# Optimization experiments

Measured on AMD Instinct MI355X. Metric: run time of the kernel, lower is better.

Reference implementation:

```python
import jax, jax.numpy as jnp
import numpy as np

N_NODES = 100000
N_EDGES = 1600000
N_GRAPHS = 256
IN_F = 64   # global_features (GNN input dim)
OUT_F = 64  # node_features (GNN output dim)


def setup_inputs() -> dict:
    key = jax.random.key(0)
    ks = jax.random.split(key, 8)
    x = jax.random.normal(ks[0], (N_NODES, IN_F), dtype=jnp.float32)
    edge_index = jax.random.randint(ks[1], (2, N_EDGES), 0, N_NODES, dtype=jnp.int64)
    batch = jnp.sort(jax.random.randint(ks[2], (N_NODES,), 0, N_GRAPHS, dtype=jnp.int64))
    # GNNLayer linear: in=global_features, out=node_features
    W_gnn = jax.random.normal(ks[3], (IN_F, OUT_F), dtype=jnp.float32) / np.sqrt(IN_F)
    b_gnn = jnp.zeros((OUT_F,), dtype=jnp.float32)
    # global_attention: Linear(node_features, 1)
    W_att = jax.random.normal(ks[4], (OUT_F, 1), dtype=jnp.float32) / np.sqrt(OUT_F)
    b_att = jnp.zeros((1,), dtype=jnp.float32)
    return {"x": x, "edge_index": edge_index, "batch": batch,
            "W_gnn": W_gnn, "b_gnn": b_gnn, "W_att": W_att, "b_att": b_att}


def reference(x, edge_index, batch, W_gnn, b_gnn, W_att, b_att):
    src, dst = edge_index[0], edge_index[1]
    # --- GNN message passing layer: aggregate neighbor features, transform ---
    agg = jax.ops.segment_sum(x[src], dst, num_segments=N_NODES)  # [N, IN_F]
    h = jax.nn.relu((x + agg) @ W_gnn + b_gnn)                    # [N, OUT_F]
    # --- attention scores + scatter softmax over batch segments ---
    scores = (h @ W_att + b_att)[:, 0]                            # [N]
    seg_max = jax.ops.segment_max(scores, batch, num_segments=N_GRAPHS)
    e = jnp.exp(scores - seg_max[batch])
    denom = jax.ops.segment_sum(e, batch, num_segments=N_GRAPHS)
    w = e / denom[batch]                                          # [N]
    # --- weighted scatter-add pooling ---
    out = jax.ops.segment_sum(w[:, None] * h, batch, num_segments=N_GRAPHS)
    return out  # [N_GRAPHS, OUT_F]
```

## Files before the change

### kernel.cpp

```cpp
#include <hip/hip_runtime.h>

#define N_NODES  100000
#define N_EDGES  1600000
#define N_GRAPHS 256
#define F        64

#define CHUNK    8192
#define NCHUNK   196
#define GBN      128
#define NB2      782
#define EDGE_CAP 2560

__device__ __forceinline__ unsigned short f2bf(float f) {
    unsigned int u = __float_as_uint(f);
    u += 0x7FFFu + ((u >> 16) & 1u);
    return (unsigned short)(u >> 16);
}
__global__ __launch_bounds__(256) void cast_kernel(
        const float* __restrict__ x, unsigned short* __restrict__ xh) {
    int i = blockIdx.x * 256 + threadIdx.x;
    float4 v = ((const float4*)x)[i];
    ushort4 o;
    o.x = f2bf(v.x); o.y = f2bf(v.y); o.z = f2bf(v.z); o.w = f2bf(v.w);
    ((ushort4*)xh)[i] = o;
}

__global__ __launch_bounds__(1024) void scatter_sort_kernel(
        const int* __restrict__ src, const int* __restrict__ dst,
        unsigned int* __restrict__ pairs, int* __restrict__ cstartT) {
    __shared__ int hist[NB2];
    __shared__ int cur[NB2];
    __shared__ int scan[1024];
    __shared__ unsigned int stage[CHUNK];
    int tid  = threadIdx.x;
    int c    = blockIdx.x;
    int base = c * CHUNK;
    int m    = min(CHUNK, N_EDGES - base);

    for (int b = tid; b < NB2; b += 1024) hist[b] = 0;
    __syncthreads();
    for (int e = tid; e < m; e += 1024)
        atomicAdd(&hist[dst[base + e] >> 7], 1);
    __syncthreads();
    scan[tid] = (tid < NB2) ? hist[tid] : 0;
    __syncthreads();
    #pragma unroll
    for (int o = 1; o < 1024; o <<= 1) {
        int u = (tid >= o) ? scan[tid - o] : 0;
        __syncthreads();
        scan[tid] += u;
        __syncthreads();
    }
    if (tid < NB2) {
        int excl = scan[tid] - hist[tid];
        cur[tid] = excl;
        cstartT[tid * NCHUNK + c] = base + excl;
    }
    if (tid == 0) cstartT[NB2 * NCHUNK + c] = base + m;
    __syncthreads();
    for (int e = tid; e < m; e += 1024) {
        int d = dst[base + e];
        int slot = atomicAdd(&cur[d >> 7], 1);
        stage[slot] = ((unsigned)(d & (GBN - 1)) << 17) | (unsigned)src[base + e];
    }
    __syncthreads();
    for (int e = tid; e < m; e += 1024)
        pairs[base + e] = stage[e];
}

__global__ __launch_bounds__(256) void compact_kernel(
        const unsigned int* __restrict__ pairs,
        const int* __restrict__ cstartT,
        int* __restrict__ eidx,
        int* __restrict__ nbeg,
        int* __restrict__ nend) {
    __shared__ int rstart[NCHUNK];
    __shared__ int rcnt[NCHUNK];
    __shared__ int roff[NCHUNK];
    __shared__ int sc[256];
    __shared__ int Etot_s;
    __shared__ unsigned int epairs[EDGE_CAP];
    __shared__ int ncnt[GBN];
    __shared__ int ncur[GBN];

    int tid   = threadIdx.x;
    int wave  = tid >> 6;
    int lane  = tid & 63;
    int b     = blockIdx.x;
    int node0 = b * GBN;
    int nn    = min(GBN, N_NODES - node0);
    int gbase = b * EDGE_CAP;

    if (tid < NCHUNK) {
        int a = cstartT[b * NCHUNK + tid];
        int n = cstartT[(b + 1) * NCHUNK + tid];
        rstart[tid] = a;
        rcnt[tid]   = n - a;
    }
    __syncthreads();
    sc[tid] = (tid < NCHUNK) ? rcnt[tid] : 0;
    __syncthreads();
    #pragma unroll
    for (int o = 1; o < 256; o <<= 1) {
        int u = (tid >= o) ? sc[tid - o] : 0;
        __syncthreads();
        sc[tid] += u;
        __syncthreads();
    }
    if (tid < NCHUNK) roff[tid] = sc[tid] - rcnt[tid];
    if (tid == 0) Etot_s = sc[NCHUNK - 1];
    __syncthreads();
    int E = Etot_s;

    for (int r = wave; r < NCHUNK; r += 4) {
        int cr = rcnt[r];
        for (int l = lane; l < cr; l += 64)
            epairs[roff[r] + l] = pairs[rstart[r] + l];
    }
    __syncthreads();

    if (tid < GBN) ncnt[tid] = 0;
    __syncthreads();
    for (int e = tid; e < E; e += 256)
        atomicAdd(&ncnt[epairs[e] >> 17], 1);
    __syncthreads();
    sc[tid] = (tid < GBN) ? ncnt[tid] : 0;
    __syncthreads();
    #pragma unroll
    for (int o = 1; o < 128; o <<= 1) {
        int u = (tid < 128 && tid >= o) ? sc[tid - o] : 0;
        __syncthreads();
        if (tid < 128) sc[tid] += u;
        __syncthreads();
    }
    if (tid < GBN) {
        int excl = sc[tid] - ncnt[tid];
        ncur[tid] = excl;
        if (tid < nn) {
            nbeg[node0 + tid] = gbase + excl;
            nend[node0 + tid] = gbase + excl + ncnt[tid];
        }
    }
    __syncthreads();
    for (int e = tid; e < E; e += 256) {
        unsigned int p = epairs[e];
        int slot = atomicAdd(&ncur[p >> 17], 1);
        eidx[gbase + slot] = (int)(p & 0x1FFFFu);
    }
}

#define NODES_PER_WAVE 25
#define GT_NWAVES  (N_NODES / NODES_PER_WAVE)
#define GT_BLOCKS  (GT_NWAVES / 4)

__device__ __forceinline__ float bfl(unsigned int u) { return __uint_as_float(u << 16); }
__device__ __forceinline__ float bfh(unsigned int u) { return __uint_as_float(u & 0xFFFF0000u); }

__global__ __launch_bounds__(256) void gather_pool_kernel(
        const unsigned short* __restrict__ xh,
        const int*   __restrict__ nbeg,
        const int*   __restrict__ nend,
        const int*   __restrict__ eidx,
        const int*   __restrict__ batch,
        const float* __restrict__ Wg,
        const float* __restrict__ bg,
        const float* __restrict__ Wa,
        const float* __restrict__ ba,
        float*       __restrict__ out_acc,
        float*       __restrict__ denom) {
    int tid  = threadIdx.x;
    int lane = tid & 63;
    int grp  = lane >> 3;
    int c    = lane & 7;
    int waveId = blockIdx.x * 4 + (tid >> 6);

    int n0 = waveId * NODES_PER_WAVE;
    if (n0 >= N_NODES) return;
    int nEnd = n0 + NODES_PER_WAVE;

    float wcol[F];
    #pragma unroll
    for (int k = 0; k < F; ++k) wcol[k] = Wg[k * F + lane];
    float bgl = bg[lane];
    float wal = Wa[lane];
    float ba0 = ba[0];

    const uint4* xh4 = (const uint4*)xh;

    int   cur_g = batch[n0];
    float accw  = 0.f;
    float denw  = 0.f;

    for (int n = n0; n < nEnd; ++n) {
        int start = nbeg[n];
        int end   = nend[n];

        float a0=0.f,a1=0.f,a2=0.f,a3=0.f,a4=0.f,a5=0.f,a6=0.f,a7=0.f;
        for (int base = start; base < end; base += 64) {
            int jmax = end - base; if (jmax > 64) jmax = 64;
            int sl = (base + lane < end) ? eidx[base + lane] : 0;
            for (int j = 0; j < jmax; j += 8) {
                int el = j + grp;
                int s  = __shfl(sl, el, 64);
                if (el < jmax) {
                    uint4 v = xh4[s * 8 + c];
                    a0 += bfl(v.x); a1 += bfh(v.x);
                    a2 += bfl(v.y); a3 += bfh(v.y);
                    a4 += bfl(v.z); a5 += bfh(v.z);
                    a6 += bfl(v.w); a7 += bfh(v.w);
                }
            }
        }
        #pragma unroll
        for (int o = 8; o <= 32; o <<= 1) {
            a0 += __shfl_xor(a0, o, 64); a1 += __shfl_xor(a1, o, 64);
            a2 += __shfl_xor(a2, o, 64); a3 += __shfl_xor(a3, o, 64);
            a4 += __shfl_xor(a4, o, 64); a5 += __shfl_xor(a5, o, 64);
            a6 += __shfl_xor(a6, o, 64); a7 += __shfl_xor(a7, o, 64);
        }
        {
            uint4 v = xh4[n * 8 + c];
            a0 += bfl(v.x); a1 += bfh(v.x);
            a2 += bfl(v.y); a3 += bfh(v.y);
            a4 += bfl(v.z); a5 += bfh(v.z);
            a6 += bfl(v.w); a7 += bfh(v.w);
        }

        float re[8] = {a0,a1,a2,a3,a4,a5,a6,a7};
        float q0=0.f,q1=0.f,q2=0.f,q3=0.f,q4=0.f,q5=0.f,q6=0.f,q7=0.f;
        #pragma unroll
        for (int k = 0; k < F; k += 8) {
            int ln = k >> 3;
            q0 += __int_as_float(__builtin_amdgcn_readlane(__float_as_int(re[0]), ln)) * wcol[k + 0];
            q1 += __int_as_float(__builtin_amdgcn_readlane(__float_as_int(re[1]), ln)) * wcol[k + 1];
            q2 += __int_as_float(__builtin_amdgcn_readlane(__float_as_int(re[2]), ln)) * wcol[k + 2];
            q3 += __int_as_float(__builtin_amdgcn_readlane(__float_as_int(re[3]), ln)) * wcol[k + 3];
            q4 += __int_as_float(__builtin_amdgcn_readlane(__float_as_int(re[4]), ln)) * wcol[k + 4];
            q5 += __int_as_float(__builtin_amdgcn_readlane(__float_as_int(re[5]), ln)) * wcol[k + 5];
            q6 += __int_as_float(__builtin_amdgcn_readlane(__float_as_int(re[6]), ln)) * wcol[k + 6];
            q7 += __int_as_float(__builtin_amdgcn_readlane(__float_as_int(re[7]), ln)) * wcol[k + 7];
        }
        float hv = ((q0 + q1) + (q2 + q3)) + ((q4 + q5) + (q6 + q7)) + bgl;
        hv = hv > 0.f ? hv : 0.f;

        float p = hv * wal;
        #pragma unroll
        for (int o = 32; o > 0; o >>= 1)
            p += __shfl_down(p, o, 64);
        float s = __int_as_float(__builtin_amdgcn_readlane(__float_as_int(p), 0)) + ba0;
        float e = __expf(s);

        int g = batch[n];
        if (g != cur_g) {
            atomicAdd(&out_acc[cur_g * F + lane], accw);
            if (lane == 0) atomicAdd(&denom[cur_g], denw);
            accw = 0.f; denw = 0.f; cur_g = g;
        }
        accw += e * hv;
        denw += e;
    }
    atomicAdd(&out_acc[cur_g * F + lane], accw);
    if (lane == 0) atomicAdd(&denom[cur_g], denw);
}

__global__ __launch_bounds__(256) void finalize_kernel(
        float* __restrict__ out, const float* __restrict__ denom) {
    int i = blockIdx.x * 256 + threadIdx.x;
    if (i >= N_GRAPHS * F) return;
    float d = denom[i >> 6];
    out[i] = (d > 0.f) ? out[i] / d : 0.f;
}

extern "C" void kernel_launch(void* const* d_in, const int* in_sizes, int n_in,
                              void* d_out, int out_size, void* d_ws, size_t ws_size,
                              hipStream_t stream) {
    const float* x     = (const float*)d_in[0];
    const int*   ei    = (const int*)d_in[1];
    const int*   batch = (const int*)d_in[2];
    const float* Wg    = (const float*)d_in[3];
    const float* bg    = (const float*)d_in[4];
    const float* Wa    = (const float*)d_in[5];
    const float* ba    = (const float*)d_in[6];
    float* out = (float*)d_out;

    const int* src = ei;
    const int* dst = ei + N_EDGES;

    char* ws = (char*)d_ws;
    unsigned short* xh      = (unsigned short*)(ws);
    unsigned int*   pairs   = (unsigned int*)(ws + 12800000);
    int*            cstartT = (int*)(ws + 19200000);
    int*            eidx    = (int*)(ws + 19814144);
    int*            nbeg    = (int*)(ws + 27821824);
    int*            nend    = (int*)(ws + 28221824);
    float*          denom   = (float*)(ws + 28621824);

    hipMemsetAsync(out,   0, (size_t)N_GRAPHS * F * sizeof(float), stream);
    hipMemsetAsync(denom, 0, N_GRAPHS * sizeof(float), stream);

    cast_kernel        <<<(N_NODES * F / 4) / 256, 256, 0, stream>>>(x, xh);
    scatter_sort_kernel<<<NCHUNK, 1024, 0, stream>>>(src, dst, pairs, cstartT);
    compact_kernel     <<<NB2, 256, 0, stream>>>(pairs, cstartT, eidx, nbeg, nend);
    gather_pool_kernel <<<GT_BLOCKS, 256, 0, stream>>>(
        xh, nbeg, nend, eidx, batch, Wg, bg, Wa, ba, out, denom);
    finalize_kernel    <<<(N_GRAPHS * F + 255) / 256, 256, 0, stream>>>(out, denom);
}
```

Before: 209.6 us.

## Merge launches: fuse cast into sort, last-block finalize, widen compact blocks

Merges the bf16 cast, the output/denominator zeroing and the edge bucket sort into one prep kernel that assigns extra blocks to the cast work. Folds the finalize step into the gather-pool kernel using a last-block-done atomic counter. Widens compact_kernel to 512 threads. This removes two memsets and two kernel launches and lets the cast overlap with the sort, at the cost of a global atomic counter and a serial tail finalize run by one block.

```diff
diff --git a/kernel.cpp b/kernel.cpp
--- a/kernel.cpp
+++ b/kernel.cpp
@@ -11,33 +11,50 @@
 #define NB2      782
 #define EDGE_CAP 2560
 
+#define CAST_ELEMS   (N_NODES * F / 4)
+#define CAST_BLOCKS  ((CAST_ELEMS + 1023) / 1024)
+#define PREP_BLOCKS  (NCHUNK + CAST_BLOCKS)
+
 __device__ __forceinline__ unsigned short f2bf(float f) {
     unsigned int u = __float_as_uint(f);
     u += 0x7FFFu + ((u >> 16) & 1u);
     return (unsigned short)(u >> 16);
 }
-__global__ __launch_bounds__(256) void cast_kernel(
-        const float* __restrict__ x, unsigned short* __restrict__ xh) {
-    int i = blockIdx.x * 256 + threadIdx.x;
-    float4 v = ((const float4*)x)[i];
-    ushort4 o;
-    o.x = f2bf(v.x); o.y = f2bf(v.y); o.z = f2bf(v.z); o.w = f2bf(v.w);
-    ((ushort4*)xh)[i] = o;
-}
-
-__global__ __launch_bounds__(1024) void scatter_sort_kernel(
+
+__global__ __launch_bounds__(1024) void prep_kernel(
+        const float* __restrict__ x, unsigned short* __restrict__ xh,
         const int* __restrict__ src, const int* __restrict__ dst,
-        unsigned int* __restrict__ pairs, int* __restrict__ cstartT) {
+        unsigned int* __restrict__ pairs, int* __restrict__ cstartT,
+        float* __restrict__ out, float* __restrict__ denom, int* __restrict__ done) {
+    int tid = threadIdx.x;
+    int b   = blockIdx.x;
+
+    if (b >= NCHUNK) {
+        int ci = b - NCHUNK;
+        if (ci == 0) {
+            for (int i = tid; i < N_GRAPHS * F; i += 1024) out[i] = 0.f;
+            if (tid < N_GRAPHS) denom[tid] = 0.f;
+            if (tid == 0) *done = 0;
+        }
+        int i = ci * 1024 + tid;
+        if (i < CAST_ELEMS) {
+            float4 v = ((const float4*)x)[i];
+            ushort4 o;
+            o.x = f2bf(v.x); o.y = f2bf(v.y); o.z = f2bf(v.z); o.w = f2bf(v.w);
+            ((ushort4*)xh)[i] = o;
+        }
+        return;
+    }
+
     __shared__ int hist[NB2];
     __shared__ int cur[NB2];
     __shared__ int scan[1024];
     __shared__ unsigned int stage[CHUNK];
-    int tid  = threadIdx.x;
-    int c    = blockIdx.x;
+    int c    = b;
     int base = c * CHUNK;
     int m    = min(CHUNK, N_EDGES - base);
 
-    for (int b = tid; b < NB2; b += 1024) hist[b] = 0;
+    for (int k = tid; k < NB2; k += 1024) hist[k] = 0;
     __syncthreads();
     for (int e = tid; e < m; e += 1024)
         atomicAdd(&hist[dst[base + e] >> 7], 1);
@@ -68,7 +85,7 @@
         pairs[base + e] = stage[e];
 }
 
-__global__ __launch_bounds__(256) void compact_kernel(
+__global__ __launch_bounds__(512) void compact_kernel(
         const unsigned int* __restrict__ pairs,
         const int* __restrict__ cstartT,
         int* __restrict__ eidx,
@@ -98,13 +115,13 @@
         rcnt[tid]   = n - a;
     }
     __syncthreads();
-    sc[tid] = (tid < NCHUNK) ? rcnt[tid] : 0;
+    if (tid < 256) sc[tid] = (tid < NCHUNK) ? rcnt[tid] : 0;
     __syncthreads();
     #pragma unroll
     for (int o = 1; o < 256; o <<= 1) {
-        int u = (tid >= o) ? sc[tid - o] : 0;
-        __syncthreads();
-        sc[tid] += u;
+        int u = (tid < 256 && tid >= o) ? sc[tid - o] : 0;
+        __syncthreads();
+        if (tid < 256) sc[tid] += u;
         __syncthreads();
     }
     if (tid < NCHUNK) roff[tid] = sc[tid] - rcnt[tid];
@@ -112,7 +129,7 @@
     __syncthreads();
     int E = Etot_s;
 
-    for (int r = wave; r < NCHUNK; r += 4) {
+    for (int r = wave; r < NCHUNK; r += 8) {
         int cr = rcnt[r];
         for (int l = lane; l < cr; l += 64)
             epairs[roff[r] + l] = pairs[rstart[r] + l];
@@ -121,10 +138,10 @@
 
     if (tid < GBN) ncnt[tid] = 0;
     __syncthreads();
-    for (int e = tid; e < E; e += 256)
+    for (int e = tid; e < E; e += 512)
         atomicAdd(&ncnt[epairs[e] >> 17], 1);
     __syncthreads();
-    sc[tid] = (tid < GBN) ? ncnt[tid] : 0;
+    if (tid < 128) sc[tid] = ncnt[tid];
     __syncthreads();
     #pragma unroll
     for (int o = 1; o < 128; o <<= 1) {
@@ -142,7 +159,7 @@
         }
     }
     __syncthreads();
-    for (int e = tid; e < E; e += 256) {
+    for (int e = tid; e < E; e += 512) {
         unsigned int p = epairs[e];
         int slot = atomicAdd(&ncur[p >> 17], 1);
         eidx[gbase + slot] = (int)(p & 0x1FFFFu);
@@ -167,15 +184,15 @@
         const float* __restrict__ Wa,
         const float* __restrict__ ba,
         float*       __restrict__ out_acc,
-        float*       __restrict__ denom) {
+        float*       __restrict__ denom,
+        int*         __restrict__ done) {
     int tid  = threadIdx.x;
     int lane = tid & 63;
     int grp  = lane >> 3;
     int c    = lane & 7;
     int waveId = blockIdx.x * 4 + (tid >> 6);
 
-    int n0 = waveId * NODES_PER_WAVE;
-    if (n0 >= N_NODES) return;
+    int n0   = waveId * NODES_PER_WAVE;
     int nEnd = n0 + NODES_PER_WAVE;
 
     float wcol[F];
@@ -261,14 +278,28 @@
     }
     atomicAdd(&out_acc[cur_g * F + lane], accw);
     if (lane == 0) atomicAdd(&denom[cur_g], denw);
-}
-
-__global__ __launch_bounds__(256) void finalize_kernel(
-        float* __restrict__ out, const float* __restrict__ denom) {
-    int i = blockIdx.x * 256 + threadIdx.x;
-    if (i >= N_GRAPHS * F) return;
-    float d = denom[i >> 6];
-    out[i] = (d > 0.f) ? out[i] / d : 0.f;
+
+    __shared__ int fin;
+    __shared__ float dinv[N_GRAPHS];
+    __syncthreads();
+    if (tid == 0) {
+        __threadfence();
+        int prev = atomicAdd(done, 1);
+        fin = (prev == GT_BLOCKS - 1) ? 1 : 0;
+    }
+    __syncthreads();
+    if (fin) {
+        __threadfence();
+        if (tid < N_GRAPHS) {
+            float d = atomicAdd(&denom[tid], 0.0f);
+            dinv[tid] = (d > 0.f) ? 1.0f / d : 0.f;
+        }
+        __syncthreads();
+        for (int i = tid; i < N_GRAPHS * F; i += 256) {
+            float v = atomicAdd(&out_acc[i], 0.0f);
+            out_acc[i] = v * dinv[i >> 6];
+        }
+    }
 }
 
 extern "C" void kernel_launch(void* const* d_in, const int* in_sizes, int n_in,
@@ -294,14 +325,11 @@
     int*            nbeg    = (int*)(ws + 27821824);
     int*            nend    = (int*)(ws + 28221824);
     float*          denom   = (float*)(ws + 28621824);
-
-    hipMemsetAsync(out,   0, (size_t)N_GRAPHS * F * sizeof(float), stream);
-    hipMemsetAsync(denom, 0, N_GRAPHS * sizeof(float), stream);
-
-    cast_kernel        <<<(N_NODES * F / 4) / 256, 256, 0, stream>>>(x, xh);
-    scatter_sort_kernel<<<NCHUNK, 1024, 0, stream>>>(src, dst, pairs, cstartT);
-    compact_kernel     <<<NB2, 256, 0, stream>>>(pairs, cstartT, eidx, nbeg, nend);
-    gather_pool_kernel <<<GT_BLOCKS, 256, 0, stream>>>(
-        xh, nbeg, nend, eidx, batch, Wg, bg, Wa, ba, out, denom);
-    finalize_kernel    <<<(N_GRAPHS * F + 255) / 256, 256, 0, stream>>>(out, denom);
-}
+    int*            done    = (int*)(ws + 28622848);
+
+    prep_kernel       <<<PREP_BLOCKS, 1024, 0, stream>>>(
+        x, xh, src, dst, pairs, cstartT, out, denom, done);
+    compact_kernel    <<<NB2, 512, 0, stream>>>(pairs, cstartT, eidx, nbeg, nend);
+    gather_pool_kernel<<<GT_BLOCKS, 256, 0, stream>>>(
+        xh, nbeg, nend, eidx, batch, Wg, bg, Wa, ba, out, denom, done);
+}
```

New measurement: 230.6 us. 1.1x slower.
